# Kernel tuning notes

Measured on AMD Instinct MI355X. Metric: run time of the kernel, lower is better.

The kernel has to match this reference:

```python
import jax, jax.numpy as jnp
import numpy as np

D_MODEL = 2048
N_HEADS = 16
D_HEAD = 128
BATCH = 2
SEQ = 2048


def setup_inputs() -> dict:
    key = jax.random.key(0)
    ks = jax.random.split(key, 5)
    x = jax.random.normal(ks[0], (BATCH, SEQ, D_MODEL), dtype=jnp.float32)
    # fused QKV projection: out features = d_model + 2*d_head
    W_qkv = jax.random.normal(ks[1], (D_MODEL, D_MODEL + 2 * D_HEAD), dtype=jnp.float32) * (D_MODEL ** -0.5)
    b_qkv = jax.random.normal(ks[2], (D_MODEL + 2 * D_HEAD,), dtype=jnp.float32) * 0.02
    W_out = jax.random.normal(ks[3], (D_MODEL, D_MODEL), dtype=jnp.float32) * (D_MODEL ** -0.5)
    b_out = jax.random.normal(ks[4], (D_MODEL,), dtype=jnp.float32) * 0.02
    return {"x": x, "W_qkv": W_qkv, "b_qkv": b_qkv, "W_out": W_out, "b_out": b_out}


def reference(x, W_qkv, b_qkv, W_out, b_out):
    B, S, _ = x.shape
    qkv = jnp.einsum('bsd,de->bse', x, W_qkv) + b_qkv
    q, k, v = jnp.split(qkv, [D_MODEL, D_MODEL + D_HEAD], axis=-1)
    # q: [B, H, S, Dh]; k, v: single shared head [B, S, Dh] (MQA broadcast)
    q = q.reshape(B, S, N_HEADS, D_HEAD).transpose(0, 2, 1, 3)
    scale = 1.0 / jnp.sqrt(jnp.float32(D_HEAD))
    # scores: [B, H, S, S] -- shared K broadcast across heads
    scores = jnp.einsum('bhqd,bkd->bhqk', q, k) * scale
    causal = jnp.tril(jnp.ones((S, S), dtype=bool))
    scores = jnp.where(causal, scores, jnp.finfo(scores.dtype).min)
    attn = jax.nn.softmax(scores, axis=-1)
    out = jnp.einsum('bhqk,bkd->bhqd', attn, v)  # shared V broadcast
    out = out.transpose(0, 2, 1, 3).reshape(B, S, D_MODEL)
    return jnp.einsum('bsd,de->bse', out, W_out) + b_out
```

## Files before the change

### kernel.cpp

```cpp
#include <hip/hip_runtime.h>

#define D_MODEL 2048
#define QKVC 2304
#define DH 128
#define NH 16
#define BATCH 2
#define SEQ 2048
#define MROWS (BATCH*SEQ)

typedef __attribute__((ext_vector_type(4))) float f32x4;
typedef __attribute__((ext_vector_type(16))) float f32x16;
typedef __attribute__((ext_vector_type(8))) short s16x8;
typedef __attribute__((ext_vector_type(8))) __bf16 bf16x8;
typedef __attribute__((ext_vector_type(4))) unsigned int u32x4;

static __device__ __forceinline__ unsigned short f2bf(float f) {
  unsigned int u = __builtin_bit_cast(unsigned int, f);
  u += 0x7fff + ((u >> 16) & 1);
  return (unsigned short)(u >> 16);
}

static __device__ __forceinline__ unsigned int pkbf(float a, float b) {
  unsigned short x = __builtin_bit_cast(unsigned short, (__bf16)a);
  unsigned short y = __builtin_bit_cast(unsigned short, (__bf16)b);
  return (unsigned int)x | ((unsigned int)y << 16);
}

static __device__ __forceinline__ f32x4 mfma16(s16x8 a, s16x8 b, f32x4 c) {
  return __builtin_amdgcn_mfma_f32_16x16x32_bf16(
      __builtin_bit_cast(bf16x8, a), __builtin_bit_cast(bf16x8, b), c, 0, 0, 0);
}

static __device__ __forceinline__ f32x16 mfma32(s16x8 a, s16x8 b, f32x16 c) {
  return __builtin_amdgcn_mfma_f32_32x32x16_bf16(
      __builtin_bit_cast(bf16x8, a), __builtin_bit_cast(bf16x8, b), c, 0, 0, 0);
}

typedef const __attribute__((address_space(1))) void gvoid_t;
typedef __attribute__((address_space(3))) void svoid_t;

static __device__ __forceinline__ void gload_lds16(const void* g, void* l) {
  __builtin_amdgcn_global_load_lds((gvoid_t*)g, (svoid_t*)l, 16, 0, 0);
}

__global__ void cvt_bf16_kernel(const float* __restrict__ in,
                                unsigned short* __restrict__ out, int n4) {
  int i = blockIdx.x * blockDim.x + threadIdx.x;
  int stride = gridDim.x * blockDim.x;
  for (int idx = i; idx < n4; idx += stride) {
    float4 v = ((const float4*)in)[idx];
    ushort4 o;
    o.x = f2bf(v.x); o.y = f2bf(v.y); o.z = f2bf(v.z); o.w = f2bf(v.w);
    ((ushort4*)out)[idx] = o;
  }
}

__global__ void transpose_cvt_kernel(const float* __restrict__ in,
                                     unsigned short* __restrict__ out,
                                     int R, int C) {
  __shared__ float tile[32][33];
  int c0 = blockIdx.x * 32, r0 = blockIdx.y * 32;
  int tx = threadIdx.x, ty = threadIdx.y;
#pragma unroll
  for (int i = 0; i < 4; ++i)
    tile[ty + i*8][tx] = in[(size_t)(r0 + ty + i*8) * C + c0 + tx];
  __syncthreads();
#pragma unroll
  for (int i = 0; i < 4; ++i)
    out[(size_t)(c0 + ty + i*8) * R + r0 + tx] = f2bf(tile[tx][ty + i*8]);
}

__global__ void transpose_v_kernel(const unsigned short* __restrict__ qkv,
                                   unsigned short* __restrict__ VT) {
  __shared__ unsigned short tile[32][33];
  int s0 = blockIdx.x * 32, d0 = blockIdx.y * 32, b = blockIdx.z;
  int tx = threadIdx.x, ty = threadIdx.y;
#pragma unroll
  for (int i = 0; i < 4; ++i)
    tile[ty + i*8][tx] =
        qkv[(size_t)(b*SEQ + s0 + ty + i*8) * QKVC + (D_MODEL + DH) + d0 + tx];
  __syncthreads();
#pragma unroll
  for (int i = 0; i < 4; ++i)
    VT[(size_t)(b*DH + d0 + ty + i*8) * SEQ + s0 + tx] = tile[tx][ty + i*8];
}

template<int OUT_F32>
__global__ __launch_bounds__(256, 2)
void gemm_bt_kernel(const unsigned short* __restrict__ A,
                    const unsigned short* __restrict__ BT,
                    const float* __restrict__ bias,
                    void* __restrict__ Cout,
                    int M, int N, int K) {
  __shared__ unsigned short Al[128*32];
  __shared__ unsigned short Bl[128*32];
  int tid = threadIdx.x;
  int lane = tid & 63, wave = tid >> 6;
  int m0 = blockIdx.y * 128, n0 = blockIdx.x * 128;
  int wr = wave >> 1, wc = wave & 1;
  int fr = lane & 15, fq = lane >> 4;
  f32x4 acc[4][4] = {};

  int c0 = wave * 2;
  int kcol = (lane & 3) * 8;
  int rsub = (lane >> 2);

  for (int k0 = 0; k0 < K; k0 += 32) {
#pragma unroll
    for (int i = 0; i < 2; ++i) {
      int c = c0 + i;
      int row = c*16 + rsub;
      gload_lds16(A  + (size_t)(m0 + row)*K + k0 + kcol, (char*)Al + c*1024);
      gload_lds16(BT + (size_t)(n0 + row)*K + k0 + kcol, (char*)Bl + c*1024);
    }
    __syncthreads();
    s16x8 af[4], bfr[4];
#pragma unroll
    for (int m = 0; m < 4; ++m)
      af[m] = *(const s16x8*)&Al[(wr*64 + m*16 + fr)*32 + fq*8];
#pragma unroll
    for (int n = 0; n < 4; ++n)
      bfr[n] = *(const s16x8*)&Bl[(wc*64 + n*16 + fr)*32 + fq*8];
#pragma unroll
    for (int m = 0; m < 4; ++m)
#pragma unroll
      for (int n = 0; n < 4; ++n)
        acc[m][n] = mfma16(af[m], bfr[n], acc[m][n]);
    __syncthreads();
  }

#pragma unroll
  for (int n = 0; n < 4; ++n) {
    int col = n0 + wc*64 + n*16 + fr;
    float bv = bias[col];
#pragma unroll
    for (int m = 0; m < 4; ++m) {
      int rowb = m0 + wr*64 + m*16 + fq*4;
#pragma unroll
      for (int j = 0; j < 4; ++j) {
        float v = acc[m][n][j] + bv;
        if (OUT_F32) ((float*)Cout)[(size_t)(rowb + j)*N + col] = v;
        else ((unsigned short*)Cout)[(size_t)(rowb + j)*N + col] = f2bf(v);
      }
    }
  }
}

__global__ __launch_bounds__(256, 2)
void mqa_attn_kernel(const unsigned short* __restrict__ qkv,
                     const unsigned short* __restrict__ VT,
                     unsigned short* __restrict__ O) {
  __shared__ unsigned short Kl[2][64*128];
  __shared__ unsigned short Vl[2][128*64];
  int qt = (gridDim.x - 1) - blockIdx.x;
  int h = blockIdx.y, b = blockIdx.z;
  int tid = threadIdx.x;
  int lane = tid & 63, wid = tid >> 6;
  int fr = lane & 31, hi = lane >> 5;
  int q0 = qt*128 + wid*32;
  const float scale = 0.08838834764831845f;

  s16x8 qf[8];
  {
    const unsigned short* qb =
        qkv + (size_t)(b*SEQ + q0 + fr)*QKVC + h*DH + hi*8;
#pragma unroll
    for (int s = 0; s < 8; ++s) qf[s] = *(const s16x8*)(qb + s*16);
  }

  f32x16 oacc[4] = {};
  float m_r = -3.0e38f, l_r = 0.f;

  int nkb = 2*(qt + 1);
  int last_act = (q0 + 31) >> 6;

#define STAGE(kb_, buf_) do {                                              \
    int kv0_ = (kb_)*64;                                                   \
    _Pragma("unroll")                                                      \
    for (int i_ = 0; i_ < 4; ++i_) {                                       \
      int idx_ = i_*256 + tid;                                             \
      int r_ = idx_ >> 4, c_ = idx_ & 15;                                  \
      gload_lds16(qkv + (size_t)(b*SEQ + kv0_ + r_)*QKVC + D_MODEL         \
                      + ((c_ ^ (r_ & 7)) * 8),                             \
                  (char*)&Kl[buf_][0] + (size_t)idx_*16);                  \
      int d_ = idx_ >> 3, c2_ = idx_ & 7;                                  \
      gload_lds16(VT + (size_t)(b*DH + d_)*SEQ + kv0_ + ((c2_ ^ (d_ & 7))*8), \
                  (char*)&Vl[buf_][0] + (size_t)idx_*16);                  \
    }                                                                      \
  } while (0)

  STAGE(0, 0);
  __syncthreads();

  for (int kb = 0; kb < nkb; ++kb) {
    int cur = kb & 1;
    if (kb + 1 < nkb) STAGE(kb + 1, cur ^ 1);

    if (kb <= last_act) {
      const unsigned short* Kb = &Kl[cur][0];
      const unsigned short* Vb = &Vl[cur][0];
      int kv0 = kb*64;

      f32x16 sfr[2] = {};
#pragma unroll
      for (int t = 0; t < 2; ++t) {
        int row = t*32 + fr;
#pragma unroll
        for (int s = 0; s < 8; ++s) {
          int cc = (s*2 + hi) ^ (fr & 7);
          s16x8 kf = *(const s16x8*)&Kb[row*128 + cc*8];
          sfr[t] = mfma32(kf, qf[s], sfr[t]);
        }
      }

      bool need_mask = (kv0 + 63 > q0);
      int q = q0 + fr;
#pragma unroll
      for (int t = 0; t < 2; ++t)
#pragma unroll
        for (int r = 0; r < 16; ++r) {
          float v = sfr[t][r] * scale;
          if (need_mask) {
            int kv = kv0 + t*32 + (r & 3) + 8*(r >> 2) + 4*hi;
            if (kv > q) v = -1.0e30f;
          }
          sfr[t][r] = v;
        }

      float pm = sfr[0][0];
#pragma unroll
      for (int t = 0; t < 2; ++t)
#pragma unroll
        for (int r = 0; r < 16; ++r) pm = fmaxf(pm, sfr[t][r]);
      pm = fmaxf(pm, __shfl_xor(pm, 32));

      bool stable = __all(pm <= m_r + 8.0f) != 0;
      float fac = 1.0f;
      if (!stable) { fac = __expf(m_r - fmaxf(m_r, pm)); m_r = fmaxf(m_r, pm); }

      float rs = 0.f;
#pragma unroll
      for (int t = 0; t < 2; ++t)
#pragma unroll
        for (int r = 0; r < 16; ++r) {
          float p = __expf(sfr[t][r] - m_r);
          sfr[t][r] = p;
          rs += p;
        }
      rs += __shfl_xor(rs, 32);
      l_r = l_r * fac + rs;

      if (!stable) {
#pragma unroll
        for (int r = 0; r < 16; ++r) {
          int src = (r & 3) + 8*(r >> 2) + 4*hi;
          float fv = __shfl(fac, src);
#pragma unroll
          for (int n2 = 0; n2 < 4; ++n2) oacc[n2][r] *= fv;
        }
      }

#pragma unroll
      for (int t = 0; t < 2; ++t) {
        s16x8 pa[2];
#pragma unroll
        for (int ks = 0; ks < 2; ++ks) {
          unsigned int X0 = pkbf(sfr[t][8*ks+0], sfr[t][8*ks+1]);
          unsigned int X1 = pkbf(sfr[t][8*ks+2], sfr[t][8*ks+3]);
          unsigned int Y0 = pkbf(sfr[t][8*ks+4], sfr[t][8*ks+5]);
          unsigned int Y1 = pkbf(sfr[t][8*ks+6], sfr[t][8*ks+7]);
          unsigned int s0 = __shfl_xor(hi ? X0 : Y0, 32);
          unsigned int s1 = __shfl_xor(hi ? X1 : Y1, 32);
          u32x4 pw;
          pw[0] = hi ? s0 : X0;
          pw[1] = hi ? s1 : X1;
          pw[2] = hi ? Y0 : s0;
          pw[3] = hi ? Y1 : s1;
          pa[ks] = __builtin_bit_cast(s16x8, pw);
        }
#pragma unroll
        for (int n2 = 0; n2 < 4; ++n2) {
          int d = n2*32 + fr;
#pragma unroll
          for (int ks = 0; ks < 2; ++ks) {
            int cc = (t*4 + ks*2 + hi) ^ (d & 7);
            s16x8 vf = *(const s16x8*)&Vb[d*64 + cc*8];
            oacc[n2] = mfma32(pa[ks], vf, oacc[n2]);
          }
        }
      }
    }
    __syncthreads();
  }

  float invl = 1.0f / l_r;
#pragma unroll
  for (int r = 0; r < 16; ++r) {
    int qrow = (r & 3) + 8*(r >> 2) + 4*hi;
    float iv = __shfl(invl, qrow);
    size_t rowoff = (size_t)(b*SEQ + q0 + qrow)*D_MODEL + h*DH;
#pragma unroll
    for (int n2 = 0; n2 < 4; ++n2)
      O[rowoff + n2*32 + fr] = f2bf(oacc[n2][r] * iv);
  }
#undef STAGE
}

extern "C" void kernel_launch(void* const* d_in, const int* in_sizes, int n_in,
                              void* d_out, int out_size, void* d_ws, size_t ws_size,
                              hipStream_t stream) {
  const float* x     = (const float*)d_in[0];
  const float* W_qkv = (const float*)d_in[1];
  const float* b_qkv = (const float*)d_in[2];
  const float* W_out = (const float*)d_in[3];
  const float* b_out = (const float*)d_in[4];
  float* out = (float*)d_out;

  unsigned short* x_bf = (unsigned short*)d_ws;
  unsigned short* WqT  = x_bf + (size_t)MROWS * D_MODEL;
  unsigned short* WoT  = WqT  + (size_t)QKVC * D_MODEL;
  unsigned short* qkvb = WoT  + (size_t)D_MODEL * D_MODEL;
  unsigned short* VTb  = qkvb + (size_t)MROWS * QKVC;
  unsigned short* Ob   = VTb  + (size_t)BATCH * DH * SEQ;

  dim3 tb(32, 8);
  cvt_bf16_kernel<<<2048, 256, 0, stream>>>(x, x_bf, (MROWS * D_MODEL) / 4);
  transpose_cvt_kernel<<<dim3(QKVC/32, D_MODEL/32), tb, 0, stream>>>(W_qkv, WqT, D_MODEL, QKVC);
  transpose_cvt_kernel<<<dim3(D_MODEL/32, D_MODEL/32), tb, 0, stream>>>(W_out, WoT, D_MODEL, D_MODEL);

  gemm_bt_kernel<0><<<dim3(QKVC/128, MROWS/128), 256, 0, stream>>>(
      x_bf, WqT, b_qkv, qkvb, MROWS, QKVC, D_MODEL);

  transpose_v_kernel<<<dim3(SEQ/32, DH/32, BATCH), tb, 0, stream>>>(qkvb, VTb);

  mqa_attn_kernel<<<dim3(SEQ/128, NH, BATCH), 256, 0, stream>>>(qkvb, VTb, Ob);

  gemm_bt_kernel<1><<<dim3(D_MODEL/128, MROWS/128), 256, 0, stream>>>(
      Ob, WoT, b_out, out, MROWS, D_MODEL, D_MODEL);
}
```

Measured before the change: 223.8 us.

## Pair causal query tiles per block and use exp2-based softmax in MQA attention

The attention kernel now uses 128-thread blocks over 64-row query tiles. Each block processes two tiles, pairing a late tile with an early one (31-pi and pi), so the causal work is balanced across blocks and no wasted K/V iterations remain. The softmax folds the scale into an exp2 constant, raises the lazy-rescale threshold, and uses tree reductions, and s_setprio is raised around the MFMA sections. The K LDS swizzle widens to 16 entries to cut bank conflicts. In exchange, each block runs fewer waves, so there is less intra-block parallelism and more blocks have to share each CU.

```diff
diff --git a/kernel.cpp b/kernel.cpp
--- a/kernel.cpp
+++ b/kernel.cpp
@@ -146,42 +146,27 @@
   }
 }
 
-__global__ __launch_bounds__(256, 2)
+__global__ __launch_bounds__(128)
 void mqa_attn_kernel(const unsigned short* __restrict__ qkv,
                      const unsigned short* __restrict__ VT,
                      unsigned short* __restrict__ O) {
   __shared__ unsigned short Kl[2][64*128];
   __shared__ unsigned short Vl[2][128*64];
-  int qt = (gridDim.x - 1) - blockIdx.x;
+  int pi = blockIdx.x;
   int h = blockIdx.y, b = blockIdx.z;
   int tid = threadIdx.x;
   int lane = tid & 63, wid = tid >> 6;
   int fr = lane & 31, hi = lane >> 5;
-  int q0 = qt*128 + wid*32;
-  const float scale = 0.08838834764831845f;
-
-  s16x8 qf[8];
-  {
-    const unsigned short* qb =
-        qkv + (size_t)(b*SEQ + q0 + fr)*QKVC + h*DH + hi*8;
-#pragma unroll
-    for (int s = 0; s < 8; ++s) qf[s] = *(const s16x8*)(qb + s*16);
-  }
-
-  f32x16 oacc[4] = {};
-  float m_r = -3.0e38f, l_r = 0.f;
-
-  int nkb = 2*(qt + 1);
-  int last_act = (q0 + 31) >> 6;
+  const float C = 0.12751688f;
 
 #define STAGE(kb_, buf_) do {                                              \
     int kv0_ = (kb_)*64;                                                   \
     _Pragma("unroll")                                                      \
-    for (int i_ = 0; i_ < 4; ++i_) {                                       \
-      int idx_ = i_*256 + tid;                                             \
+    for (int i_ = 0; i_ < 8; ++i_) {                                       \
+      int idx_ = i_*128 + tid;                                             \
       int r_ = idx_ >> 4, c_ = idx_ & 15;                                  \
       gload_lds16(qkv + (size_t)(b*SEQ + kv0_ + r_)*QKVC + D_MODEL         \
-                      + ((c_ ^ (r_ & 7)) * 8),                             \
+                      + ((c_ ^ (r_ & 15)) * 8),                            \
                   (char*)&Kl[buf_][0] + (size_t)idx_*16);                  \
       int d_ = idx_ >> 3, c2_ = idx_ & 7;                                  \
       gload_lds16(VT + (size_t)(b*DH + d_)*SEQ + kv0_ + ((c2_ ^ (d_ & 7))*8), \
@@ -189,64 +174,87 @@
     }                                                                      \
   } while (0)
 
-  STAGE(0, 0);
-  __syncthreads();
-
-  for (int kb = 0; kb < nkb; ++kb) {
-    int cur = kb & 1;
-    if (kb + 1 < nkb) STAGE(kb + 1, cur ^ 1);
-
-    if (kb <= last_act) {
+  for (int phase = 0; phase < 2; ++phase) {
+    int qt = phase ? pi : (31 - pi);
+    int q0 = qt*64 + wid*32;
+
+    s16x8 qf[8];
+    {
+      const unsigned short* qb =
+          qkv + (size_t)(b*SEQ + q0 + fr)*QKVC + h*DH + hi*8;
+#pragma unroll
+      for (int s = 0; s < 8; ++s) qf[s] = *(const s16x8*)(qb + s*16);
+    }
+
+    f32x16 oacc[4] = {};
+    float m_r = -1.0e30f, l_r = 0.f;
+
+    int nkb = qt + 1;
+    STAGE(0, 0);
+    __syncthreads();
+
+    for (int kb = 0; kb < nkb; ++kb) {
+      int cur = kb & 1;
+      if (kb + 1 < nkb) STAGE(kb + 1, cur ^ 1);
+
       const unsigned short* Kb = &Kl[cur][0];
       const unsigned short* Vb = &Vl[cur][0];
       int kv0 = kb*64;
 
       f32x16 sfr[2] = {};
+      __builtin_amdgcn_s_setprio(1);
 #pragma unroll
       for (int t = 0; t < 2; ++t) {
         int row = t*32 + fr;
 #pragma unroll
         for (int s = 0; s < 8; ++s) {
-          int cc = (s*2 + hi) ^ (fr & 7);
+          int cc = (s*2 + hi) ^ (fr & 15);
           s16x8 kf = *(const s16x8*)&Kb[row*128 + cc*8];
           sfr[t] = mfma32(kf, qf[s], sfr[t]);
         }
       }
-
-      bool need_mask = (kv0 + 63 > q0);
-      int q = q0 + fr;
+      __builtin_amdgcn_s_setprio(0);
+
+      if (kb == qt) {
+        int q = q0 + fr;
+#pragma unroll
+        for (int t = 0; t < 2; ++t)
+#pragma unroll
+          for (int r = 0; r < 16; ++r) {
+            int kv = kv0 + t*32 + (r & 3) + 8*(r >> 2) + 4*hi;
+            if (kv > q) sfr[t][r] = -1.0e30f;
+          }
+      }
+
+      float mx[8];
+#pragma unroll
+      for (int r = 0; r < 8; ++r)
+        mx[r] = fmaxf(fmaxf(sfr[0][r], sfr[0][r+8]),
+                      fmaxf(sfr[1][r], sfr[1][r+8]));
+      float pm = fmaxf(fmaxf(fmaxf(mx[0], mx[4]), fmaxf(mx[1], mx[5])),
+                       fmaxf(fmaxf(mx[2], mx[6]), fmaxf(mx[3], mx[7])));
+      pm = fmaxf(pm, __shfl_xor(pm, 32));
+
+      bool stable = __all(pm - m_r <= 90.0f) != 0;
+      float fac = 1.0f;
+      if (!stable) {
+        float mnew = fmaxf(m_r, pm);
+        fac = exp2f((m_r - mnew) * C);
+        m_r = mnew;
+      }
+      float mC = m_r * C;
 #pragma unroll
       for (int t = 0; t < 2; ++t)
 #pragma unroll
-        for (int r = 0; r < 16; ++r) {
-          float v = sfr[t][r] * scale;
-          if (need_mask) {
-            int kv = kv0 + t*32 + (r & 3) + 8*(r >> 2) + 4*hi;
-            if (kv > q) v = -1.0e30f;
-          }
-          sfr[t][r] = v;
-        }
-
-      float pm = sfr[0][0];
-#pragma unroll
-      for (int t = 0; t < 2; ++t)
-#pragma unroll
-        for (int r = 0; r < 16; ++r) pm = fmaxf(pm, sfr[t][r]);
-      pm = fmaxf(pm, __shfl_xor(pm, 32));
-
-      bool stable = __all(pm <= m_r + 8.0f) != 0;
-      float fac = 1.0f;
-      if (!stable) { fac = __expf(m_r - fmaxf(m_r, pm)); m_r = fmaxf(m_r, pm); }
-
-      float rs = 0.f;
-#pragma unroll
-      for (int t = 0; t < 2; ++t)
-#pragma unroll
-        for (int r = 0; r < 16; ++r) {
-          float p = __expf(sfr[t][r] - m_r);
-          sfr[t][r] = p;
-          rs += p;
-        }
+        for (int r = 0; r < 16; ++r)
+          sfr[t][r] = exp2f(__builtin_fmaf(sfr[t][r], C, -mC));
+
+      float sm[8];
+#pragma unroll
+      for (int r = 0; r < 8; ++r)
+        sm[r] = (sfr[0][r] + sfr[0][r+8]) + (sfr[1][r] + sfr[1][r+8]);
+      float rs = ((sm[0]+sm[1]) + (sm[2]+sm[3]))
+               + ((sm[4]+sm[5]) + (sm[6]+sm[7]));
       rs += __shfl_xor(rs, 32);
       l_r = l_r * fac + rs;
 
@@ -278,6 +286,7 @@
           pw[3] = hi ? Y1 : s1;
           pa[ks] = __builtin_bit_cast(s16x8, pw);
         }
+        __builtin_amdgcn_s_setprio(1);
 #pragma unroll
         for (int n2 = 0; n2 < 4; ++n2) {
           int d = n2*32 + fr;
@@ -288,20 +297,22 @@
             oacc[n2] = mfma32(pa[ks], vf, oacc[n2]);
           }
         }
-      }
-    }
-    __syncthreads();
-  }
-
-  float invl = 1.0f / l_r;
-#pragma unroll
-  for (int r = 0; r < 16; ++r) {
-    int qrow = (r & 3) + 8*(r >> 2) + 4*hi;
-    float iv = __shfl(invl, qrow);
-    size_t rowoff = (size_t)(b*SEQ + q0 + qrow)*D_MODEL + h*DH;
-#pragma unroll
-    for (int n2 = 0; n2 < 4; ++n2)
-      O[rowoff + n2*32 + fr] = f2bf(oacc[n2][r] * iv);
+        __builtin_amdgcn_s_setprio(0);
+      }
+
+      __syncthreads();
+    }
+
+    float invl = 1.0f / l_r;
+#pragma unroll
+    for (int r = 0; r < 16; ++r) {
+      int qrow = (r & 3) + 8*(r >> 2) + 4*hi;
+      float iv = __shfl(invl, qrow);
+      size_t rowoff = (size_t)(b*SEQ + q0 + qrow)*D_MODEL + h*DH;
+#pragma unroll
+      for (int n2 = 0; n2 < 4; ++n2)
+        O[rowoff + n2*32 + fr] = f2bf(oacc[n2][r] * iv);
+    }
   }
 #undef STAGE
 }
@@ -333,7 +344,7 @@
 
   transpose_v_kernel<<<dim3(SEQ/32, DH/32, BATCH), tb, 0, stream>>>(qkvb, VTb);
 
-  mqa_attn_kernel<<<dim3(SEQ/128, NH, BATCH), 256, 0, stream>>>(qkvb, VTb, Ob);
+  mqa_attn_kernel<<<dim3(16, NH, BATCH), 128, 0, stream>>>(qkvb, VTb, Ob);
 
   gemm_bt_kernel<1><<<dim3(D_MODEL/128, MROWS/128), 256, 0, stream>>>(
       Ob, WoT, b_out, out, MROWS, D_MODEL, D_MODEL);
```

Result: slower. 231.2 us (+3.3%).
